# Performance work log

Hardware: AMD Instinct MI355X
Metric: run time of the kernel (lower is better)

The kernel has to match this reference:

```python
import jax, jax.numpy as jnp
import numpy as np
import math


def _bandwidth(d):
    # gz = 2*Gamma((d+1)/2)/Gamma(d/2); use lgamma for numerical stability.
    gz = 2.0 * math.exp(math.lgamma(0.5 * (d + 1)) - math.lgamma(0.5 * d))
    return 1.0 / (2.0 * gz * gz)


def _kernel_mean(xa, xb, gamma):
    # mean over the [Na, Nb] RBF kernel matrix, squared distance via matmul identity
    sq = (jnp.sum(xa * xa, axis=1)[:, None]
          + jnp.sum(xb * xb, axis=1)[None, :]
          - 2.0 * (xa @ xb.T))
    sq = jnp.maximum(sq, 0.0)  # guard tiny negatives from the identity
    return jnp.mean(jnp.exp(-gamma * sq))


def setup_inputs() -> dict:
    key = jax.random.key(0)
    k1, k2 = jax.random.split(key)
    x1 = jax.random.normal(k1, (8192, 128), dtype=jnp.float32)
    x2 = jax.random.normal(k2, (8192, 128), dtype=jnp.float32)
    return {"x1": x1, "x2": x2}


def reference(x1, x2):
    g1 = _bandwidth(x1.shape[1])
    g2 = _bandwidth(x2.shape[1])
    m11 = _kernel_mean(x1, x1, g1)
    m22 = _kernel_mean(x2, x2, g2)
    m12 = _kernel_mean(x1, x2, g1)
    return jnp.sqrt(m11 - 2.0 * m12 + m22)
```

## Files before the change

kernel.cpp:

```cpp
#include <hip/hip_runtime.h>
#include <cmath>

#define D 128
#define BM 128
#define BK 64
#define LOG2E 1.4426950408889634

typedef __attribute__((ext_vector_type(8))) _Float16 f16x8;
typedef __attribute__((ext_vector_type(4))) float f32x4;
typedef __attribute__((ext_vector_type(2))) float f32x2;

__device__ __forceinline__ void async_cp16(const void* g, void* l) {
    __builtin_amdgcn_global_load_lds(
        (__attribute__((address_space(1))) void*)g,
        (__attribute__((address_space(3))) void*)l, 16, 0, 0);
}

__global__ __launch_bounds__(256) void prep_kernel(
    const float* __restrict__ x1, const float* __restrict__ x2,
    _Float16* __restrict__ xh, float* __restrict__ El,
    double* __restrict__ acc, float gl, int N) {
    int tid = threadIdx.x;
    if (blockIdx.x == 0 && tid < 64) acc[tid] = 0.0;
    int r = blockIdx.x * 16 + (tid >> 4);
    if (r >= 2 * N) return;
    int l = tid & 15;
    const float* row = (r < N) ? x1 + (size_t)r * D : x2 + (size_t)(r - N) * D;
    float4 v0 = ((const float4*)row)[l * 2];
    float4 v1 = ((const float4*)row)[l * 2 + 1];
    float v[8] = {v0.x, v0.y, v0.z, v0.w, v1.x, v1.y, v1.z, v1.w};
    float p = 0.f;
    _Float16 h8[8];
#pragma unroll
    for (int j = 0; j < 8; ++j) {
        p = fmaf(v[j], v[j], p);
        h8[j] = (_Float16)v[j];
    }
    *(uint4*)(xh + (size_t)r * D + l * 8) = *(uint4*)h8;
#pragma unroll
    for (int off = 8; off; off >>= 1) p += __shfl_down(p, off, 16);
    if (l == 0) El[r] = gl * p;
}

__global__ __launch_bounds__(256, 4) void mmd_mfma_kernel(
    const _Float16* __restrict__ xh, const float* __restrict__ El,
    double* __restrict__ acc, float c2l, int N) {
    __shared__ float4 smem[2048];

    int t = blockIdx.x;
    int bi = (int)((sqrtf(8.0f * t + 1.0f) - 1.0f) * 0.5f);
    while ((bi + 1) * (bi + 2) / 2 <= t) ++bi;
    while (bi * (bi + 1) / 2 > t) --bi;
    int bj = t - bi * (bi + 1) / 2;

    int half = N / BM;
    float w = (bi == bj) ? 1.0f : 2.0f;
    if ((bi < half) != (bj < half)) w = -2.0f;
    int aBase = bi * BM, bBase = bj * BM;

    int tid = threadIdx.x;
    int lane = tid & 63, wave = tid >> 6;
    int quad = lane >> 4, l16 = lane & 15;
    int wrow = (wave & 1) * 64, wcol = (wave >> 1) * 64;

    f32x4 C[4][4];
#pragma unroll
    for (int i = 0; i < 4; ++i)
#pragma unroll
        for (int j = 0; j < 4; ++j) C[i][j] = {0.f, 0.f, 0.f, 0.f};

    for (int c = 0; c < 2; ++c) {
        if (c) __syncthreads();
#pragma unroll
        for (int r = 0; r < 2; ++r) {
            int rowBase = r ? bBase : aBase;
#pragma unroll
            for (int i = 0; i < 4; ++i) {
                int slot = i * 256 + tid;
                int row = slot >> 3, g = slot & 7;
                int kc4 = g ^ (row & 7);
                const void* gp = xh + ((size_t)(rowBase + row) * D + c * BK + kc4 * 8);
                async_cp16(gp, &smem[r * 1024 + slot]);
            }
        }
        __syncthreads();
#pragma unroll
        for (int s = 0; s < 2; ++s) {
            int kc4 = s * 4 + quad;
            f16x8 a[4], b[4];
#pragma unroll
            for (int u = 0; u < 4; ++u) {
                int ar = wrow + u * 16 + l16;
                a[u] = *(const f16x8*)&smem[ar * 8 + (kc4 ^ (ar & 7))];
                int br = wcol + u * 16 + l16;
                b[u] = *(const f16x8*)&smem[1024 + br * 8 + (kc4 ^ (br & 7))];
            }
#pragma unroll
            for (int ti = 0; ti < 4; ++ti)
#pragma unroll
                for (int tj = 0; tj < 4; ++tj)
                    C[ti][tj] = __builtin_amdgcn_mfma_f32_16x16x32_f16(a[ti], b[tj], C[ti][tj], 0, 0, 0);
        }
    }

    int arow0 = aBase + wrow + quad * 4;
    int bcol0 = bBase + wcol + l16;
    float4 ea4[4];
#pragma unroll
    for (int ti = 0; ti < 4; ++ti) ea4[ti] = *(const float4*)&El[arow0 + ti * 16];
    f32x2 cc = {c2l, c2l};
    float lsum = 0.f;
#pragma unroll
    for (int tj = 0; tj < 4; ++tj) {
        float eb = El[bcol0 + tj * 16];
        f32x2 p = {0.f, 0.f};
#pragma unroll
        for (int ti = 0; ti < 4; ++ti) {
            f32x4 d = C[ti][tj];
            f32x2 a01 = cc * f32x2{d.x, d.y} + f32x2{ea4[ti].x, ea4[ti].y};
            f32x2 a23 = cc * f32x2{d.z, d.w} + f32x2{ea4[ti].z, ea4[ti].w};
            f32x2 e;
            e.x = __builtin_amdgcn_exp2f(a01.x);
            e.y = __builtin_amdgcn_exp2f(a01.y);
            f32x2 e2;
            e2.x = __builtin_amdgcn_exp2f(a23.x);
            e2.y = __builtin_amdgcn_exp2f(a23.y);
            p += e + e2;
        }
        lsum = fmaf(p.x + p.y, __builtin_amdgcn_exp2f(eb), lsum);
    }
    double ds = (double)lsum * (double)w;
#pragma unroll
    for (int off = 32; off; off >>= 1) ds += __shfl_down(ds, off);
    __syncthreads();
    double* red = (double*)smem;
    if (lane == 0) red[wave] = ds;
    __syncthreads();
    if (tid == 0)
        atomicAdd(&acc[(bi + bj) & 63], red[0] + red[1] + red[2] + red[3]);
}

__global__ __launch_bounds__(64) void mmd_finalize_kernel(
    const double* __restrict__ acc, float* __restrict__ out, int N) {
    int l = threadIdx.x;
    double v = acc[l];
#pragma unroll
    for (int off = 32; off; off >>= 1) v += __shfl_down(v, off);
    if (l == 0) {
        double nn = (double)N * (double)N;
        double s = v / nn;
        out[0] = (float)sqrt(s > 0.0 ? s : 0.0);
    }
}

extern "C" void kernel_launch(void* const* d_in, const int* in_sizes, int n_in,
                              void* d_out, int out_size, void* d_ws, size_t ws_size,
                              hipStream_t stream) {
    const float* x1 = (const float*)d_in[0];
    const float* x2 = (const float*)d_in[1];
    int N = in_sizes[0] / D;

    double* acc = (double*)d_ws;
    float* El = (float*)((char*)d_ws + 8192);
    _Float16* xh = (_Float16*)((char*)d_ws + 73728);

    double lg = lgamma(0.5 * (D + 1)) - lgamma(0.5 * D);
    double gz = 2.0 * exp(lg);
    double gamma = 1.0 / (2.0 * gz * gz);
    float gl = (float)(-gamma * LOG2E);
    float c2l = (float)(2.0 * gamma * LOG2E);

    prep_kernel<<<(2 * N + 15) / 16, 256, 0, stream>>>(x1, x2, xh, El, acc, gl, N);

    int nt2 = 2 * N / BM;
    int nblocks = nt2 * (nt2 + 1) / 2;
    mmd_mfma_kernel<<<nblocks, 256, 0, stream>>>(xh, El, acc, c2l, N);

    mmd_finalize_kernel<<<1, 64, 0, stream>>>(acc, (float*)d_out, N);
}
```

Before: 110.7 us.

## Shrink column tile to 64 rows and remap triangular block indexing

Changes the output tile from 128x128 to 128x64, so each block covers one row tile against one of the two half-width column tiles in the lower triangle, and rebuilds the triangular index decode and diagonal/cross weights to match. Shared memory drops and the occupancy hint rises from 4 to 5 blocks per SIMD, aiming for better latency hiding and finer load balance. The cost is that each block loads its A tile for half the compute, so arithmetic intensity falls and about twice as many blocks and atomics are issued.

```diff
diff --git a/kernel.cpp b/kernel.cpp
--- a/kernel.cpp
+++ b/kernel.cpp
@@ -3,6 +3,7 @@
 
 #define D 128
 #define BM 128
+#define BN 64
 #define BK 64
 #define LOG2E 1.4426950408889634
 
@@ -42,63 +43,71 @@
     if (l == 0) El[r] = gl * p;
 }
 
-__global__ __launch_bounds__(256, 4) void mmd_mfma_kernel(
+__global__ __launch_bounds__(256, 5) void mmd_mfma_kernel(
     const _Float16* __restrict__ xh, const float* __restrict__ El,
     double* __restrict__ acc, float c2l, int N) {
-    __shared__ float4 smem[2048];
+    __shared__ float4 smem[1536];
 
     int t = blockIdx.x;
-    int bi = (int)((sqrtf(8.0f * t + 1.0f) - 1.0f) * 0.5f);
-    while ((bi + 1) * (bi + 2) / 2 <= t) ++bi;
-    while (bi * (bi + 1) / 2 > t) --bi;
-    int bj = t - bi * (bi + 1) / 2;
+    int bi = (int)((sqrtf(4.0f * t + 1.0f) - 1.0f) * 0.5f);
+    while ((bi + 1) * (bi + 2) <= t) ++bi;
+    while (bi * (bi + 1) > t) --bi;
+    int bj = t - bi * (bi + 1);
 
-    int half = N / BM;
-    float w = (bi == bj) ? 1.0f : 2.0f;
-    if ((bi < half) != (bj < half)) w = -2.0f;
-    int aBase = bi * BM, bBase = bj * BM;
+    int halfM = N / BM;
+    int halfN = N / BN;
+    float w = ((bj >> 1) == bi) ? 1.0f : 2.0f;
+    if ((bi < halfM) != (bj < halfN)) w = -2.0f;
+    int aBase = bi * BM, bBase = bj * BN;
 
     int tid = threadIdx.x;
     int lane = tid & 63, wave = tid >> 6;
     int quad = lane >> 4, l16 = lane & 15;
-    int wrow = (wave & 1) * 64, wcol = (wave >> 1) * 64;
+    int wrow = (wave & 1) * 64, wcol = (wave >> 1) * 32;
 
-    f32x4 C[4][4];
+    f32x4 C[4][2];
 #pragma unroll
     for (int i = 0; i < 4; ++i)
 #pragma unroll
-        for (int j = 0; j < 4; ++j) C[i][j] = {0.f, 0.f, 0.f, 0.f};
+        for (int j = 0; j < 2; ++j) C[i][j] = {0.f, 0.f, 0.f, 0.f};
 
     for (int c = 0; c < 2; ++c) {
         if (c) __syncthreads();
 #pragma unroll
-        for (int r = 0; r < 2; ++r) {
-            int rowBase = r ? bBase : aBase;
+        for (int i = 0; i < 4; ++i) {
+            int slot = i * 256 + tid;
+            int row = slot >> 3;
+            int kc4 = (slot & 7) ^ (row & 7);
+            const void* gp = xh + ((size_t)(aBase + row) * D + c * BK + kc4 * 8);
+            async_cp16(gp, &smem[slot]);
+        }
 #pragma unroll
-            for (int i = 0; i < 4; ++i) {
-                int slot = i * 256 + tid;
-                int row = slot >> 3, g = slot & 7;
-                int kc4 = g ^ (row & 7);
-                const void* gp = xh + ((size_t)(rowBase + row) * D + c * BK + kc4 * 8);
-                async_cp16(gp, &smem[r * 1024 + slot]);
-            }
+        for (int i = 0; i < 2; ++i) {
+            int slot = i * 256 + tid;
+            int row = slot >> 3;
+            int kc4 = (slot & 7) ^ (row & 7);
+            const void* gp = xh + ((size_t)(bBase + row) * D + c * BK + kc4 * 8);
+            async_cp16(gp, &smem[1024 + slot]);
         }
         __syncthreads();
 #pragma unroll
         for (int s = 0; s < 2; ++s) {
             int kc4 = s * 4 + quad;
-            f16x8 a[4], b[4];
+            f16x8 a[4], b[2];
 #pragma unroll
             for (int u = 0; u < 4; ++u) {
                 int ar = wrow + u * 16 + l16;
                 a[u] = *(const f16x8*)&smem[ar * 8 + (kc4 ^ (ar & 7))];
-                int br = wcol + u * 16 + l16;
-                b[u] = *(const f16x8*)&smem[1024 + br * 8 + (kc4 ^ (br & 7))];
+            }
+#pragma unroll
+            for (int v = 0; v < 2; ++v) {
+                int br = wcol + v * 16 + l16;
+                b[v] = *(const f16x8*)&smem[1024 + br * 8 + (kc4 ^ (br & 7))];
             }
 #pragma unroll
             for (int ti = 0; ti < 4; ++ti)
 #pragma unroll
-                for (int tj = 0; tj < 4; ++tj)
+                for (int tj = 0; tj < 2; ++tj)
                     C[ti][tj] = __builtin_amdgcn_mfma_f32_16x16x32_f16(a[ti], b[tj], C[ti][tj], 0, 0, 0);
         }
     }
@@ -111,7 +120,7 @@
     f32x2 cc = {c2l, c2l};
     float lsum = 0.f;
 #pragma unroll
-    for (int tj = 0; tj < 4; ++tj) {
+    for (int tj = 0; tj < 2; ++tj) {
         float eb = El[bcol0 + tj * 16];
         f32x2 p = {0.f, 0.f};
 #pragma unroll
@@ -172,8 +181,8 @@
 
     prep_kernel<<<(2 * N + 15) / 16, 256, 0, stream>>>(x1, x2, xh, El, acc, gl, N);
 
-    int nt2 = 2 * N / BM;
-    int nblocks = nt2 * (nt2 + 1) / 2;
+    int ntM = 2 * N / BM;
+    int nblocks = ntM * (ntM + 1);
     mmd_mfma_kernel<<<nblocks, 256, 0, stream>>>(xh, El, acc, c2l, N);
 
     mmd_finalize_kernel<<<1, 64, 0, stream>>>(acc, (float*)d_out, N);
```

Result: slower. 122.0 us (+10.2%).
